# Performance work log

Hardware: AMD Instinct MI355X
Metric: run time of the kernel (lower is better)

The kernel has to match this reference:

```python
import jax, jax.numpy as jnp
import numpy as np

B, S, H = 128, 1000, 256


def setup_inputs() -> dict:
    key = jax.random.key(0)
    ks = jax.random.split(key, 15)
    sc = 1.0 / np.sqrt(H)
    f = lambda k, shape: (jax.random.normal(k, shape, jnp.float32) * sc)
    return dict(
        static_hidden=jax.random.normal(ks[0], (B, S, H), jnp.float32),
        state_embedding=jax.random.normal(ks[1], (B, 1, H), jnp.float32),
        decoder_hidden=jax.random.normal(ks[2], (B, 1, H), jnp.float32),
        target_hidden=jax.random.normal(ks[3], (B, 1, H), jnp.float32),
        last_hh=jax.random.normal(ks[4], (1, B, H), jnp.float32),
        W_ih=f(ks[5], (3 * H, H)),
        W_hh=f(ks[6], (3 * H, H)),
        b_ih=f(ks[7], (3 * H,)),
        b_hh=f(ks[8], (3 * H,)),
        v_attn_enc=f(ks[9], (H,)),
        W_attn_enc=f(ks[10], (H, 2 * H)),
        v_attn_tgt=f(ks[11], (H,)),
        W_attn_tgt=f(ks[12], (H, 2 * H)),
        v_ptr=f(ks[13], (H,)),
        W_ptr=f(ks[14], (H, 3 * H)),
    )


def _attention(static, dec, v, W):
    # static: [B,S,H], dec: [B,1,H] -> softmax attention over S
    hid = jnp.concatenate([static, jnp.broadcast_to(dec, static.shape)], axis=2)  # [B,S,2H]
    t = jnp.tanh(jnp.einsum('hk,bsk->bhs', W, hid))  # [B,H,S]
    return jax.nn.softmax(jnp.einsum('h,bhs->bs', v, t), axis=1)  # [B,S]


def _gru_step(x, h, Wih, Whh, bih, bhh):
    # single-layer single-step torch GRU semantics; x,h: [B,H]
    gi = x @ Wih.T + bih
    gh = h @ Whh.T + bhh
    ir, iz, ig = jnp.split(gi, 3, axis=-1)
    hr, hz, hg = jnp.split(gh, 3, axis=-1)
    r = jax.nn.sigmoid(ir + hr)
    z = jax.nn.sigmoid(iz + hz)
    n = jnp.tanh(ig + r * hg)
    return (1.0 - z) * n + z * h


def _pointer_branch(static, state_emb, attn, v, W):
    context = jnp.einsum('bs,bsh->bh', attn, static)[:, None, :]  # [B,1,H]
    energy = jnp.concatenate(
        [static,
         jnp.broadcast_to(context, static.shape),
         jnp.broadcast_to(state_emb, static.shape)], axis=2)  # [B,S,3H]
    return jnp.einsum('h,bhs->bs', v, jnp.tanh(jnp.einsum('hk,bsk->bhs', W, energy)))


def reference(static_hidden, state_embedding, decoder_hidden, target_hidden, last_hh,
              W_ih, W_hh, b_ih, b_hh,
              v_attn_enc, W_attn_enc, v_attn_tgt, W_attn_tgt, v_ptr, W_ptr):
    # GRU step (dropout is identity in eval / p=0.0)
    h_new = _gru_step(decoder_hidden[:, 0, :], last_hh[0], W_ih, W_hh, b_ih, b_hh)
    rnn_out = h_new[:, None, :]  # [B,1,H]
    last_hh_new = h_new[None]    # [1,B,H]

    enc_attn = _attention(static_hidden, rnn_out, v_attn_enc, W_attn_enc)
    probs = _pointer_branch(static_hidden, state_embedding, enc_attn, v_ptr, W_ptr)

    tgt_attn = _attention(static_hidden, target_hidden, v_attn_tgt, W_attn_tgt)
    # NOTE: original code reuses self.v / self.W (not v_target/W_taret) for the
    # target branch energy -- replicated faithfully.
    probs_target = _pointer_branch(static_hidden, state_embedding, tgt_attn, v_ptr, W_ptr)

    return (5.0 * probs + probs_target, last_hh_new)
```

## Files before the change

kernel.cpp:

```cpp
#include <hip/hip_runtime.h>
#include <hip/hip_bf16.h>
#include <stdint.h>
#include <stddef.h>

#define Bn 128
#define Sn 1000
#define SP 1024
#define Hn 256

typedef __bf16 bf16;
typedef __bf16 bf16x8 __attribute__((ext_vector_type(8)));
typedef __bf16 bf16x4 __attribute__((ext_vector_type(4)));
typedef float  f32x16 __attribute__((ext_vector_type(16)));

typedef __attribute__((address_space(1))) const unsigned int* gas1;
typedef __attribute__((address_space(3))) unsigned int* las3;

__device__ __forceinline__ float fast_tanh(float x){
  return 1.0f - 2.0f / (__expf(2.0f * x) + 1.0f);
}
__device__ __forceinline__ float fast_sigmoid(float x){
  return 1.0f / (1.0f + __expf(-x));
}

__global__ void k0w(const float* __restrict__ We, const float* __restrict__ Wt,
                    const float* __restrict__ Wp, bf16* __restrict__ Wcb,
                    const float* __restrict__ dec, const float* __restrict__ lhh,
                    const float* __restrict__ tgt, const float* __restrict__ se,
                    float* __restrict__ xT, float* __restrict__ hT,
                    float* __restrict__ tT, float* __restrict__ sT){
  int blk = blockIdx.x, t = threadIdx.x;
  if (blk < 768){
    int tt = blk*256 + t;
    int r = tt >> 8, c = tt & 255;
    float val;
    if (r < 256)       val = We[r*512 + c];
    else if (r < 512)  val = Wt[(r-256)*512 + c];
    else               val = Wp[(r-512)*768 + c];
    Wcb[tt] = (bf16)val;
  } else {
    int idx = blk - 768;
    int a = idx >> 7, bb = idx & 127;
    const float* src = (a==0) ? dec : (a==1) ? lhh : (a==2) ? tgt : se;
    float* dst       = (a==0) ? xT  : (a==1) ? hT  : (a==2) ? tT  : sT;
    dst[t*128 + bb] = src[bb*256 + t];
  }
}

__global__ __launch_bounds__(512) void k1a_gru(
    const float* __restrict__ xT, const float* __restrict__ hT,
    const float* __restrict__ Wih, const float* __restrict__ Whh,
    const float* __restrict__ bih, const float* __restrict__ bhh,
    float* __restrict__ out_hh, float* __restrict__ hnT){
  int t = threadIdx.x;
  int g = t >> 7, b = t & 127;
  int h = blockIdx.x*4 + g;
  const float4* wir = (const float4*)(Wih + (size_t)h*256);
  const float4* wiz = (const float4*)(Wih + (size_t)(256+h)*256);
  const float4* wig = (const float4*)(Wih + (size_t)(512+h)*256);
  const float4* whr = (const float4*)(Whh + (size_t)h*256);
  const float4* whz = (const float4*)(Whh + (size_t)(256+h)*256);
  const float4* whg = (const float4*)(Whh + (size_t)(512+h)*256);
  float air=0.f, aiz=0.f, aig=0.f, ahr=0.f, ahz=0.f, ahg=0.f;
  #pragma unroll 2
  for (int kq=0; kq<64; kq++){
    float4 vir = wir[kq], viz = wiz[kq], vig = wig[kq];
    float4 vhr = whr[kq], vhz = whz[kq], vhg = whg[kq];
    #pragma unroll
    for (int e=0;e<4;e++){
      int k = kq*4 + e;
      float xv = xT[k*128 + b];
      float hv = hT[k*128 + b];
      air += (&vir.x)[e]*xv; aiz += (&viz.x)[e]*xv; aig += (&vig.x)[e]*xv;
      ahr += (&vhr.x)[e]*hv; ahz += (&vhz.x)[e]*hv; ahg += (&vhg.x)[e]*hv;
    }
  }
  air += bih[h];      ahr += bhh[h];
  aiz += bih[256+h];  ahz += bhh[256+h];
  aig += bih[512+h];  ahg += bhh[512+h];
  float r = fast_sigmoid(air + ahr);
  float z = fast_sigmoid(aiz + ahz);
  float n = fast_tanh(aig + r*ahg);
  float hprev = hT[h*128 + b];
  float hnew = (1.f - z)*n + z*hprev;
  out_hh[b*256 + h] = hnew;
  hnT[h*128 + b] = hnew;
}

__global__ __launch_bounds__(512) void k1c_dots(
    const float* __restrict__ hnT, const float* __restrict__ tT,
    const float* __restrict__ sT,
    const float* __restrict__ We, const float* __restrict__ Wt,
    const float* __restrict__ Wp,
    float* __restrict__ dEnc, float* __restrict__ dTgt, float* __restrict__ c3){
  int t = threadIdx.x;
  int g = t >> 7, b = t & 127;
  int vr = blockIdx.x*4 + g;
  int var = vr >> 8, h = vr & 255;
  const float* wrow; const float* X; float* dst;
  if (var == 0)      { wrow = We + (size_t)h*512 + 256; X = hnT; dst = dEnc; }
  else if (var == 1) { wrow = Wt + (size_t)h*512 + 256; X = tT;  dst = dTgt; }
  else               { wrow = Wp + (size_t)h*768 + 512; X = sT;  dst = c3; }
  const float4* w4 = (const float4*)wrow;
  float acc = 0.f;
  #pragma unroll 2
  for (int kq=0; kq<64; kq++){
    float4 wv = w4[kq];
    #pragma unroll
    for (int e=0;e<4;e++)
      acc += (&wv.x)[e] * X[(kq*4+e)*128 + b];
  }
  dst[b*256 + h] = acc;
}

__global__ __launch_bounds__(256, 2) void k2_gemm(
    const float* __restrict__ stat, const bf16* __restrict__ Wcb,
    const float* __restrict__ dEnc, const float* __restrict__ dTgt,
    const float* __restrict__ vEnc, const float* __restrict__ vTgt,
    float* __restrict__ scE, float* __restrict__ scT, bf16* __restrict__ Aptr){
  __shared__ __align__(16) bf16 As[64*256];
  __shared__ __align__(16) bf16 Bs[2][256*32];
  __shared__ float scr[2][4][64];
  int tid = threadIdx.x, w = tid>>6, l = tid&63;
  int l31 = l&31, lh = l>>5;
  int st = blockIdx.x, b = blockIdx.y;

  int bnb = w*16 + (l>>2);
  int bg  = l&3;

  {
    int am = tid>>2, agk = tid&3;
    bool aValid = (st*64 + am) < Sn;
    const float4* aSrc4 = (const float4*)(stat + ((size_t)b*Sn + st*64 + am)*Hn);
    #pragma unroll
    for (int i=0;i<8;i++){
      int G = i*4 + agk;
      float4 f0 = make_float4(0.f,0.f,0.f,0.f), f1 = f0;
      if (aValid){ f0 = aSrc4[G*2]; f1 = aSrc4[G*2+1]; }
      bf16x8 v;
      v[0]=(bf16)f0.x; v[1]=(bf16)f0.y; v[2]=(bf16)f0.z; v[3]=(bf16)f0.w;
      v[4]=(bf16)f1.x; v[5]=(bf16)f1.y; v[6]=(bf16)f1.z; v[7]=(bf16)f1.w;
      *(bf16x8*)&As[am*256 + ((G ^ (am&7))<<3)] = v;
    }
  }
  __syncthreads();

#define STAGE(it, buf) { \
  const bf16* wb_ = Wcb + (size_t)((it)>>3)*65536 + ((it)&7)*32; \
  _Pragma("unroll") \
  for (int i_=0;i_<4;i_++){ \
    int n_ = i_*64 + bnb; \
    int g_ = bg ^ ((n_>>1)&3); \
    __builtin_amdgcn_global_load_lds((gas1)(wb_ + (size_t)n_*256 + g_*8), \
        (las3)(&Bs[buf][i_*2048 + w*512]), 16, 0, 0); \
  } }

#define CHUNK(it) { \
  const bf16* bsr_ = &Bs[(it)&1][0]; \
  _Pragma("unroll") \
  for (int ks=0; ks<2; ks++){ \
    int kg_ = ks*2 + lh; \
    int G_ = ((it)&7)*4 + kg_; \
    int sa_ = (G_ ^ (l31&7))<<3; \
    bf16x8 af0 = *(const bf16x8*)&As[l31*256 + sa_]; \
    bf16x8 af1 = *(const bf16x8*)&As[(32+l31)*256 + sa_]; \
    _Pragma("unroll") \
    for (int c_=0;c_<2;c_++){ \
      int n_ = w*64 + c_*32 + l31; \
      bf16x8 wf = *(const bf16x8*)&bsr_[n_*32 + ((kg_ ^ ((n_>>1)&3))<<3)]; \
      acc[0][c_] = __builtin_amdgcn_mfma_f32_32x32x16_bf16(wf, af0, acc[0][c_], 0,0,0); \
      acc[1][c_] = __builtin_amdgcn_mfma_f32_32x32x16_bf16(wf, af1, acc[1][c_], 0,0,0); \
    } \
  } }

  STAGE(0, 0);
  STAGE(1, 1);
  __builtin_amdgcn_sched_barrier(0);
  asm volatile("s_waitcnt vmcnt(4)" ::: "memory");
  __builtin_amdgcn_sched_barrier(0);
  __builtin_amdgcn_s_barrier();
  __builtin_amdgcn_sched_barrier(0);

  float scp0[2] = {0.f,0.f}, scp1[2] = {0.f,0.f};
  f32x16 acc[2][2];

  #pragma unroll
  for (int p=0; p<3; p++){
    #pragma unroll
    for (int a=0;a<2;a++)
      #pragma unroll
      for (int c=0;c<2;c++)
        #pragma unroll
        for (int r=0;r<16;r++) acc[a][c][r] = 0.f;

    #pragma unroll
    for (int kt=0; kt<8; kt++){
      int it = p*8 + kt;
      CHUNK(it);
      if (it < 23){
        __builtin_amdgcn_sched_barrier(0);
        __builtin_amdgcn_s_barrier();
        __builtin_amdgcn_sched_barrier(0);
        if (it < 22){ STAGE(it+2, (it&1)); }
        __builtin_amdgcn_sched_barrier(0);
        if (it < 22){ asm volatile("s_waitcnt vmcnt(4)" ::: "memory"); }
        else        { asm volatile("s_waitcnt vmcnt(0)" ::: "memory"); }
        __builtin_amdgcn_sched_barrier(0);
        __builtin_amdgcn_s_barrier();
        __builtin_amdgcn_sched_barrier(0);
      }
    }

    if (p < 2){
      const float* vv = p ? vTgt : vEnc;
      const float* db = (p ? dTgt : dEnc) + b*256;
      float s0 = 0.f, s1 = 0.f;
      #pragma unroll
      for (int c=0;c<2;c++){
        int nb = w*64 + c*32 + 4*lh;
        #pragma unroll
        for (int r=0;r<16;r++){
          int n = nb + (r&3) + 8*(r>>2);
          float vdv = vv[n], ddv = db[n];
          s0 += vdv * fast_tanh(acc[0][c][r] + ddv);
          s1 += vdv * fast_tanh(acc[1][c][r] + ddv);
        }
      }
      scp0[p] = s0; scp1[p] = s1;
    }
  }

  __syncthreads();
  #pragma unroll
  for (int a=0;a<2;a++){
    int m = a*32 + l31;
    #pragma unroll
    for (int c=0;c<2;c++){
      int g0 = w*8 + c*4 + lh*2;
      bf16x8 lo, hi;
      #pragma unroll
      for (int r=0;r<8;r++){ lo[r] = (bf16)acc[a][c][r]; hi[r] = (bf16)acc[a][c][8+r]; }
      *(bf16x8*)&As[m*256 + (( g0    ^ (m&7))<<3)] = lo;
      *(bf16x8*)&As[m*256 + (((g0+1) ^ (m&7))<<3)] = hi;
    }
  }
  #pragma unroll
  for (int p2=0;p2<2;p2++){
    float v0 = scp0[p2] + __shfl_xor(scp0[p2], 32);
    float v1 = scp1[p2] + __shfl_xor(scp1[p2], 32);
    if (lh == 0){
      scr[p2][w][l31]      = v0;
      scr[p2][w][32 + l31] = v1;
    }
  }
  __syncthreads();
  if (tid < 128){
    int pp = tid>>6, m = tid&63;
    float s = scr[pp][0][m] + scr[pp][1][m] + scr[pp][2][m] + scr[pp][3][m];
    (pp ? scT : scE)[b*SP + st*64 + m] = s;
  }
  {
    int m = tid>>2, part = tid&3;
    bf16* dst = Aptr + ((size_t)(b*1024 + st*64 + m))*256 + part*64;
    #pragma unroll
    for (int i=0;i<8;i++){
      int g = (part*8 + i) ^ (m&7);
      *(bf16x8*)(dst + i*8) = *(const bf16x8*)&As[m*256 + (g<<3)];
    }
  }
#undef STAGE
#undef CHUNK
}

__global__ __launch_bounds__(1024) void k3_ctx(
    const float* __restrict__ scE, const float* __restrict__ scT,
    const float* __restrict__ stat, float* __restrict__ ctxG){
  __shared__ float attE[500], attT[500];
  __shared__ float redE[16], redT[16];
  __shared__ float4 pe4[16][64], pt4[16][64];
  int b = blockIdx.x, sg = blockIdx.y, t = threadIdx.x;
  int wid = t>>6, ln = t&63;

  float vE = (t < Sn) ? scE[b*SP + t] : -1e30f;
  float vT = (t < Sn) ? scT[b*SP + t] : -1e30f;
  float mE = vE, mT = vT;
  #pragma unroll
  for (int o=1;o<64;o<<=1){ mE=fmaxf(mE,__shfl_xor(mE,o)); mT=fmaxf(mT,__shfl_xor(mT,o)); }
  if (ln==0){ redE[wid]=mE; redT[wid]=mT; }
  __syncthreads();
  float ME=-1e30f, MT=-1e30f;
  #pragma unroll
  for (int i=0;i<16;i++){ ME=fmaxf(ME,redE[i]); MT=fmaxf(MT,redT[i]); }
  __syncthreads();
  float eE = (t < Sn) ? __expf(vE-ME) : 0.f;
  float eT = (t < Sn) ? __expf(vT-MT) : 0.f;
  float sE=eE, sT=eT;
  #pragma unroll
  for (int o=1;o<64;o<<=1){ sE+=__shfl_xor(sE,o); sT+=__shfl_xor(sT,o); }
  if (ln==0){ redE[wid]=sE; redT[wid]=sT; }
  __syncthreads();
  float SE=0.f, ST=0.f;
  #pragma unroll
  for (int i=0;i<16;i++){ SE+=redE[i]; ST+=redT[i]; }
  float invE = 1.f/SE, invT = 1.f/ST;
  if (t < 500){
    int s = sg*500 + t;
    attE[t] = __expf(scE[b*SP+s]-ME)*invE;
    attT[t] = __expf(scT[b*SP+s]-MT)*invT;
  }
  __syncthreads();

  int h4 = t & 63, rg = t >> 6;
  float4 aE = make_float4(0.f,0.f,0.f,0.f), aT = aE;
  int nrows = (rg == 15) ? 20 : 32;
  const float4* base = (const float4*)(stat + ((size_t)(b*Sn + sg*500 + rg*32))*Hn) + h4;
  #pragma unroll 4
  for (int i=0;i<nrows;i++){
    float4 f = base[(size_t)i*64];
    float wE = attE[rg*32 + i], wT = attT[rg*32 + i];
    aE.x += wE*f.x; aE.y += wE*f.y; aE.z += wE*f.z; aE.w += wE*f.w;
    aT.x += wT*f.x; aT.y += wT*f.y; aT.z += wT*f.z; aT.w += wT*f.w;
  }
  pe4[rg][h4] = aE; pt4[rg][h4] = aT;
  __syncthreads();
  if (t < 64){
    float4 s = make_float4(0.f,0.f,0.f,0.f);
    #pragma unroll
    for (int i=0;i<16;i++){
      float4 p = pe4[i][t];
      s.x+=p.x; s.y+=p.y; s.z+=p.z; s.w+=p.w;
    }
    atomicAdd(&ctxG[b*256 + t*4 + 0], s.x);
    atomicAdd(&ctxG[b*256 + t*4 + 1], s.y);
    atomicAdd(&ctxG[b*256 + t*4 + 2], s.z);
    atomicAdd(&ctxG[b*256 + t*4 + 3], s.w);
  } else if (t < 128){
    int h = t - 64;
    float4 s = make_float4(0.f,0.f,0.f,0.f);
    #pragma unroll
    for (int i=0;i<16;i++){
      float4 p = pt4[i][h];
      s.x+=p.x; s.y+=p.y; s.z+=p.z; s.w+=p.w;
    }
    atomicAdd(&ctxG[32768 + b*256 + h*4 + 0], s.x);
    atomicAdd(&ctxG[32768 + b*256 + h*4 + 1], s.y);
    atomicAdd(&ctxG[32768 + b*256 + h*4 + 2], s.z);
    atomicAdd(&ctxG[32768 + b*256 + h*4 + 3], s.w);
  }
}

__global__ __launch_bounds__(512) void k3c_c2(
    const float* __restrict__ ctxG, const float* __restrict__ Wp,
    const float* __restrict__ c3,
    float* __restrict__ cE, float* __restrict__ cT){
  __shared__ __align__(16) float ctxL[512];
  int b = blockIdx.x, t = threadIdx.x;
  ctxL[t] = ctxG[(t>>8)*32768 + b*256 + (t&255)];
  __syncthreads();
  int var = t >> 8, h = t & 255;
  const float4* w4 = (const float4*)(Wp + (size_t)h*768 + 256);
  const float4* cv = (const float4*)(&ctxL[var*256]);
  float acc = 0.f;
  #pragma unroll 4
  for (int k=0;k<64;k++){
    float4 wv = w4[k], xv = cv[k];
    acc += wv.x*xv.x + wv.y*xv.y + wv.z*xv.z + wv.w*xv.w;
  }
  (var ? cT : cE)[b*256 + h] = acc + c3[b*256 + h];
}

__global__ __launch_bounds__(256) void k4_final(
    const bf16* __restrict__ Aptr, const float* __restrict__ cE,
    const float* __restrict__ cT, const float* __restrict__ vp,
    float* __restrict__ out){
  int t = threadIdx.x;
  int st = blockIdx.x, b = blockIdx.y;
  int m = t>>2, part = t&3;
  const bf16* src = Aptr + ((size_t)(b*1024 + st*64 + m))*256 + part*64;
  const float* vpb = vp + part*64;
  const float* ceb = cE + b*256 + part*64;
  const float* ctb = cT + b*256 + part*64;
  float pe = 0.f, pt = 0.f;
  #pragma unroll
  for (int i=0;i<8;i++){
    bf16x8 av = *(const bf16x8*)(src + i*8);
    int bi = ((i>>2)<<5) + (((i>>1)&1)<<2) + ((i&1)<<4);
    float4 v0 = *(const float4*)(vpb + bi), v1 = *(const float4*)(vpb + bi + 8);
    float4 e0 = *(const float4*)(ceb + bi), e1 = *(const float4*)(ceb + bi + 8);
    float4 t0 = *(const float4*)(ctb + bi), t1 = *(const float4*)(ctb + bi + 8);
    #pragma unroll
    for (int j=0;j<4;j++){
      float a = (float)av[j];
      pe += (&v0.x)[j] * fast_tanh(a + (&e0.x)[j]);
      pt += (&v0.x)[j] * fast_tanh(a + (&t0.x)[j]);
    }
    #pragma unroll
    for (int j=0;j<4;j++){
      float a = (float)av[4+j];
      pe += (&v1.x)[j] * fast_tanh(a + (&e1.x)[j]);
      pt += (&v1.x)[j] * fast_tanh(a + (&t1.x)[j]);
    }
  }
  pe += __shfl_xor(pe,1); pe += __shfl_xor(pe,2);
  pt += __shfl_xor(pt,1); pt += __shfl_xor(pt,2);
  int s = st*64 + m;
  if (part==0 && s < Sn) out[(size_t)b*Sn + s] = 5.0f*pe + pt;
}

extern "C" void kernel_launch(void* const* d_in, const int* in_sizes, int n_in,
                              void* d_out, int out_size, void* d_ws, size_t ws_size,
                              hipStream_t stream){
  const float* stat = (const float*)d_in[0];
  const float* se   = (const float*)d_in[1];
  const float* dec  = (const float*)d_in[2];
  const float* tgt  = (const float*)d_in[3];
  const float* lhh  = (const float*)d_in[4];
  const float* Wih  = (const float*)d_in[5];
  const float* Whh  = (const float*)d_in[6];
  const float* bih  = (const float*)d_in[7];
  const float* bhh  = (const float*)d_in[8];
  const float* vEnc = (const float*)d_in[9];
  const float* WEnc = (const float*)d_in[10];
  const float* vTgt = (const float*)d_in[11];
  const float* WTgt = (const float*)d_in[12];
  const float* vPtr = (const float*)d_in[13];
  const float* WPtr = (const float*)d_in[14];
  float* out = (float*)d_out;

  char* wsp = (char*)d_ws;
  bf16*  Aptr = (bf16*)(wsp);
  bf16*  Wcb  = (bf16*)(wsp + 67108864);
  float* xT   = (float*)(wsp + 67502080);
  float* hT   = (float*)(wsp + 67633152);
  float* tT   = (float*)(wsp + 67764224);
  float* sT   = (float*)(wsp + 67895296);
  float* hnT  = (float*)(wsp + 68026368);
  float* scE  = (float*)(wsp + 68157440);
  float* scT  = (float*)(wsp + 68681728);
  float* dEnc = (float*)(wsp + 69206016);
  float* dTgt = (float*)(wsp + 69337088);
  float* c3   = (float*)(wsp + 69468160);
  float* cE   = (float*)(wsp + 69599232);
  float* cT   = (float*)(wsp + 69730304);
  float* ctxG = (float*)(wsp + 69861376);

  hipMemsetAsync(ctxG, 0, 262144, stream);
  hipLaunchKernelGGL(k0w, dim3(1280), dim3(256), 0, stream,
                     WEnc, WTgt, WPtr, Wcb, dec, lhh, tgt, se, xT, hT, tT, sT);
  hipLaunchKernelGGL(k1a_gru, dim3(64), dim3(512), 0, stream,
                     xT, hT, Wih, Whh, bih, bhh, out + Bn*Sn, hnT);
  hipLaunchKernelGGL(k1c_dots, dim3(192), dim3(512), 0, stream,
                     hnT, tT, sT, WEnc, WTgt, WPtr, dEnc, dTgt, c3);
  hipLaunchKernelGGL(k2_gemm, dim3(16, 128), dim3(256), 0, stream,
                     stat, Wcb, dEnc, dTgt, vEnc, vTgt, scE, scT, Aptr);
  hipLaunchKernelGGL(k3_ctx, dim3(128, 2), dim3(1024), 0, stream,
                     scE, scT, stat, ctxG);
  hipLaunchKernelGGL(k3c_c2, dim3(128), dim3(512), 0, stream,
                     ctxG, WPtr, c3, cE, cT);
  hipLaunchKernelGGL(k4_final, dim3(16, 128), dim3(256), 0, stream,
                     Aptr, cE, cT, vPtr, out);
}
```

Baseline: 455.2 us.

## Enlarge k2 GEMM tile to 128 rows with 8 waves and 64-wide K chunks

```diff
diff --git a/kernel.cpp b/kernel.cpp
--- a/kernel.cpp
+++ b/kernel.cpp
@@ -113,25 +113,22 @@
   dst[b*256 + h] = acc;
 }
 
-__global__ __launch_bounds__(256, 2) void k2_gemm(
+__global__ __launch_bounds__(512, 2) void k2_gemm(
     const float* __restrict__ stat, const bf16* __restrict__ Wcb,
     const float* __restrict__ dEnc, const float* __restrict__ dTgt,
     const float* __restrict__ vEnc, const float* __restrict__ vTgt,
     float* __restrict__ scE, float* __restrict__ scT, bf16* __restrict__ Aptr){
-  __shared__ __align__(16) bf16 As[64*256];
-  __shared__ __align__(16) bf16 Bs[2][256*32];
-  __shared__ float scr[2][4][64];
+  __shared__ __align__(16) bf16 Bs[2][256*64];
+  __shared__ __align__(16) bf16 As[128*256];
   int tid = threadIdx.x, w = tid>>6, l = tid&63;
   int l31 = l&31, lh = l>>5;
   int st = blockIdx.x, b = blockIdx.y;
-
-  int bnb = w*16 + (l>>2);
-  int bg  = l&3;
+  int wn = (w&3)*64, wm = (w>>2)*64;
 
   {
     int am = tid>>2, agk = tid&3;
-    bool aValid = (st*64 + am) < Sn;
-    const float4* aSrc4 = (const float4*)(stat + ((size_t)b*Sn + st*64 + am)*Hn);
+    bool aValid = (st*128 + am) < Sn;
+    const float4* aSrc4 = (const float4*)(stat + ((size_t)b*Sn + st*128 + am)*Hn);
     #pragma unroll
     for (int i=0;i<8;i++){
       int G = i*4 + agk;
@@ -146,28 +143,28 @@
   __syncthreads();
 
 #define STAGE(it, buf) { \
-  const bf16* wb_ = Wcb + (size_t)((it)>>3)*65536 + ((it)&7)*32; \
+  const bf16* wb_ = Wcb + (size_t)((it)>>2)*65536 + ((it)&3)*64; \
   _Pragma("unroll") \
   for (int i_=0;i_<4;i_++){ \
-    int n_ = i_*64 + bnb; \
-    int g_ = bg ^ ((n_>>1)&3); \
+    int n_ = i_*64 + w*8 + (l>>3); \
+    int g_ = (l&7) ^ (n_&7); \
     __builtin_amdgcn_global_load_lds((gas1)(wb_ + (size_t)n_*256 + g_*8), \
-        (las3)(&Bs[buf][i_*2048 + w*512]), 16, 0, 0); \
+        (las3)(&Bs[buf][(i_*512 + w*64)*8]), 16, 0, 0); \
   } }
 
 #define CHUNK(it) { \
   const bf16* bsr_ = &Bs[(it)&1][0]; \
   _Pragma("unroll") \
-  for (int ks=0; ks<2; ks++){ \
+  for (int ks=0; ks<4; ks++){ \
     int kg_ = ks*2 + lh; \
-    int G_ = ((it)&7)*4 + kg_; \
+    int G_  = ((it)&3)*8 + kg_; \
     int sa_ = (G_ ^ (l31&7))<<3; \
-    bf16x8 af0 = *(const bf16x8*)&As[l31*256 + sa_]; \
-    bf16x8 af1 = *(const bf16x8*)&As[(32+l31)*256 + sa_]; \
+    bf16x8 af0 = *(const bf16x8*)&As[(wm + l31)*256 + sa_]; \
+    bf16x8 af1 = *(const bf16x8*)&As[(wm + 32 + l31)*256 + sa_]; \
     _Pragma("unroll") \
     for (int c_=0;c_<2;c_++){ \
-      int n_ = w*64 + c_*32 + l31; \
-      bf16x8 wf = *(const bf16x8*)&bsr_[n_*32 + ((kg_ ^ ((n_>>1)&3))<<3)]; \
+      int n_ = wn + c_*32 + l31; \
+      bf16x8 wf = *(const bf16x8*)&bsr_[n_*64 + ((kg_ ^ (n_&7))<<3)]; \
       acc[0][c_] = __builtin_amdgcn_mfma_f32_32x32x16_bf16(wf, af0, acc[0][c_], 0,0,0); \
       acc[1][c_] = __builtin_amdgcn_mfma_f32_32x32x16_bf16(wf, af1, acc[1][c_], 0,0,0); \
     } \
@@ -194,16 +191,16 @@
         for (int r=0;r<16;r++) acc[a][c][r] = 0.f;
 
     #pragma unroll
-    for (int kt=0; kt<8; kt++){
-      int it = p*8 + kt;
+    for (int kt=0; kt<4; kt++){
+      int it = p*4 + kt;
       CHUNK(it);
-      if (it < 23){
+      if (it < 11){
         __builtin_amdgcn_sched_barrier(0);
         __builtin_amdgcn_s_barrier();
         __builtin_amdgcn_sched_barrier(0);
-        if (it < 22){ STAGE(it+2, (it&1)); }
+        if (it < 10){ STAGE(it+2, (it&1)); }
         __builtin_amdgcn_sched_barrier(0);
-        if (it < 22){ asm volatile("s_waitcnt vmcnt(4)" ::: "memory"); }
+        if (it < 10){ asm volatile("s_waitcnt vmcnt(4)" ::: "memory"); }
         else        { asm volatile("s_waitcnt vmcnt(0)" ::: "memory"); }
         __builtin_amdgcn_sched_barrier(0);
         __builtin_amdgcn_s_barrier();
@@ -217,7 +214,7 @@
       float s0 = 0.f, s1 = 0.f;
       #pragma unroll
       for (int c=0;c<2;c++){
-        int nb = w*64 + c*32 + 4*lh;
+        int nb = wn + c*32 + 4*lh;
         #pragma unroll
         for (int r=0;r<16;r++){
           int n = nb + (r&3) + 8*(r>>2);
@@ -230,13 +227,14 @@
     }
   }
 
+  float (*scr)[8][64] = (float (*)[8][64])&Bs[0][0];
   __syncthreads();
   #pragma unroll
   for (int a=0;a<2;a++){
-    int m = a*32 + l31;
+    int m = wm + a*32 + l31;
     #pragma unroll
     for (int c=0;c<2;c++){
-      int g0 = w*8 + c*4 + lh*2;
+      int g0 = (w&3)*8 + c*4 + lh*2;
       bf16x8 lo, hi;
       #pragma unroll
       for (int r=0;r<8;r++){ lo[r] = (bf16)acc[a][c][r]; hi[r] = (bf16)acc[a][c][8+r]; }
@@ -254,14 +252,16 @@
     }
   }
   __syncthreads();
-  if (tid < 128){
-    int pp = tid>>6, m = tid&63;
-    float s = scr[pp][0][m] + scr[pp][1][m] + scr[pp][2][m] + scr[pp][3][m];
-    (pp ? scT : scE)[b*SP + st*64 + m] = s;
+  if (tid < 256){
+    int pp = tid>>7, m = tid&127;
+    int grp = (m>>6)*4, mi = m&63;
+    float s = scr[pp][grp][mi] + scr[pp][grp+1][mi]
+            + scr[pp][grp+2][mi] + scr[pp][grp+3][mi];
+    (pp ? scT : scE)[b*SP + st*128 + m] = s;
   }
   {
     int m = tid>>2, part = tid&3;
-    bf16* dst = Aptr + ((size_t)(b*1024 + st*64 + m))*256 + part*64;
+    bf16* dst = Aptr + (((size_t)(b*8 + st)*128 + m))*256 + part*64;
     #pragma unroll
     for (int i=0;i<8;i++){
       int g = (part*8 + i) ^ (m&7);
@@ -369,14 +369,14 @@
   (var ? cT : cE)[b*256 + h] = acc + c3[b*256 + h];
 }
 
-__global__ __launch_bounds__(256) void k4_final(
+__global__ __launch_bounds__(512) void k4_final(
     const bf16* __restrict__ Aptr, const float* __restrict__ cE,
     const float* __restrict__ cT, const float* __restrict__ vp,
     float* __restrict__ out){
   int t = threadIdx.x;
   int st = blockIdx.x, b = blockIdx.y;
   int m = t>>2, part = t&3;
-  const bf16* src = Aptr + ((size_t)(b*1024 + st*64 + m))*256 + part*64;
+  const bf16* src = Aptr + (((size_t)(b*8 + st)*128 + m))*256 + part*64;
   const float* vpb = vp + part*64;
   const float* ceb = cE + b*256 + part*64;
   const float* ctb = cT + b*256 + part*64;
@@ -403,7 +403,7 @@
   }
   pe += __shfl_xor(pe,1); pe += __shfl_xor(pe,2);
   pt += __shfl_xor(pt,1); pt += __shfl_xor(pt,2);
-  int s = st*64 + m;
+  int s = st*128 + m;
   if (part==0 && s < Sn) out[(size_t)b*Sn + s] = 5.0f*pe + pt;
 }
 
@@ -451,12 +451,12 @@
                      xT, hT, Wih, Whh, bih, bhh, out + Bn*Sn, hnT);
   hipLaunchKernelGGL(k1c_dots, dim3(192), dim3(512), 0, stream,
                      hnT, tT, sT, WEnc, WTgt, WPtr, dEnc, dTgt, c3);
-  hipLaunchKernelGGL(k2_gemm, dim3(16, 128), dim3(256), 0, stream,
+  hipLaunchKernelGGL(k2_gemm, dim3(8, 128), dim3(512), 0, stream,
                      stat, Wcb, dEnc, dTgt, vEnc, vTgt, scE, scT, Aptr);
   hipLaunchKernelGGL(k3_ctx, dim3(128, 2), dim3(1024), 0, stream,
                      scE, scT, stat, ctxG);
   hipLaunchKernelGGL(k3c_c2, dim3(128), dim3(512), 0, stream,
                      ctxG, WPtr, c3, cE, cT);
-  hipLaunchKernelGGL(k4_final, dim3(16, 128), dim3(256), 0, stream,
+  hipLaunchKernelGGL(k4_final, dim3(8, 128), dim3(512), 0, stream,
                      Aptr, cE, cT, vPtr, out);
 }
```

After: 475.2 us. 4.4% more time.

## Triple-buffer weight tiles with interleaved loads and MFMA priority; split context kernel finer

Applied to the files above, without the earlier changes.

```diff
diff --git a/kernel.cpp b/kernel.cpp
--- a/kernel.cpp
+++ b/kernel.cpp
@@ -118,12 +118,12 @@
     const float* __restrict__ dEnc, const float* __restrict__ dTgt,
     const float* __restrict__ vEnc, const float* __restrict__ vTgt,
     float* __restrict__ scE, float* __restrict__ scT, bf16* __restrict__ Aptr){
+  __shared__ __align__(16) bf16 Bs[3][256*32];
   __shared__ __align__(16) bf16 As[64*256];
-  __shared__ __align__(16) bf16 Bs[2][256*32];
-  __shared__ float scr[2][4][64];
   int tid = threadIdx.x, w = tid>>6, l = tid&63;
   int l31 = l&31, lh = l>>5;
   int st = blockIdx.x, b = blockIdx.y;
+  int wn = w*64;
 
   int bnb = w*16 + (l>>2);
   int bg  = l&3;
@@ -145,41 +145,17 @@
   }
   __syncthreads();
 
-#define STAGE(it, buf) { \
+#define BISSUE(it, i_) { \
   const bf16* wb_ = Wcb + (size_t)((it)>>3)*65536 + ((it)&7)*32; \
-  _Pragma("unroll") \
-  for (int i_=0;i_<4;i_++){ \
-    int n_ = i_*64 + bnb; \
-    int g_ = bg ^ ((n_>>1)&3); \
-    __builtin_amdgcn_global_load_lds((gas1)(wb_ + (size_t)n_*256 + g_*8), \
-        (las3)(&Bs[buf][i_*2048 + w*512]), 16, 0, 0); \
-  } }
-
-#define CHUNK(it) { \
-  const bf16* bsr_ = &Bs[(it)&1][0]; \
-  _Pragma("unroll") \
-  for (int ks=0; ks<2; ks++){ \
-    int kg_ = ks*2 + lh; \
-    int G_ = ((it)&7)*4 + kg_; \
-    int sa_ = (G_ ^ (l31&7))<<3; \
-    bf16x8 af0 = *(const bf16x8*)&As[l31*256 + sa_]; \
-    bf16x8 af1 = *(const bf16x8*)&As[(32+l31)*256 + sa_]; \
-    _Pragma("unroll") \
-    for (int c_=0;c_<2;c_++){ \
-      int n_ = w*64 + c_*32 + l31; \
-      bf16x8 wf = *(const bf16x8*)&bsr_[n_*32 + ((kg_ ^ ((n_>>1)&3))<<3)]; \
-      acc[0][c_] = __builtin_amdgcn_mfma_f32_32x32x16_bf16(wf, af0, acc[0][c_], 0,0,0); \
-      acc[1][c_] = __builtin_amdgcn_mfma_f32_32x32x16_bf16(wf, af1, acc[1][c_], 0,0,0); \
-    } \
-  } }
-
-  STAGE(0, 0);
-  STAGE(1, 1);
-  __builtin_amdgcn_sched_barrier(0);
+  int n_ = (i_)*64 + bnb; \
+  int g_ = bg ^ ((n_>>1)&3); \
+  __builtin_amdgcn_global_load_lds((gas1)(wb_ + (size_t)n_*256 + g_*8), \
+      (las3)(&Bs[(it)%3][(i_)*2048 + w*512]), 16, 0, 0); }
+
+  BISSUE(0,0); BISSUE(0,1); BISSUE(0,2); BISSUE(0,3);
+  BISSUE(1,0); BISSUE(1,1); BISSUE(1,2); BISSUE(1,3);
   asm volatile("s_waitcnt vmcnt(4)" ::: "memory");
-  __builtin_amdgcn_sched_barrier(0);
   __builtin_amdgcn_s_barrier();
-  __builtin_amdgcn_sched_barrier(0);
 
   float scp0[2] = {0.f,0.f}, scp1[2] = {0.f,0.f};
   f32x16 acc[2][2];
@@ -196,18 +172,32 @@
     #pragma unroll
     for (int kt=0; kt<8; kt++){
       int it = p*8 + kt;
-      CHUNK(it);
-      if (it < 23){
+      const bf16* bsr = &Bs[it%3][0];
+      #pragma unroll
+      for (int sp=0; sp<2; sp++){
+        int kg = sp*2 + lh;
+        int G  = kt*4 + kg;
+        int sa = (G ^ (l31&7))<<3;
+        bf16x8 af0 = *(const bf16x8*)&As[l31*256 + sa];
+        bf16x8 af1 = *(const bf16x8*)&As[(32+l31)*256 + sa];
+        int n0 = wn + l31, n1 = wn + 32 + l31;
+        bf16x8 wf0 = *(const bf16x8*)&bsr[n0*32 + ((kg ^ ((n0>>1)&3))<<3)];
+        bf16x8 wf1 = *(const bf16x8*)&bsr[n1*32 + ((kg ^ ((n1>>1)&3))<<3)];
+        if (it < 22){ BISSUE(it+2, sp*2); BISSUE(it+2, sp*2+1); }
+        if (sp == 1){
+          if (it < 22){ asm volatile("s_waitcnt vmcnt(4)" ::: "memory"); }
+          else        { asm volatile("s_waitcnt vmcnt(0)" ::: "memory"); }
+        }
+        __builtin_amdgcn_s_barrier();
+        asm volatile("s_waitcnt lgkmcnt(0)" ::: "memory");
         __builtin_amdgcn_sched_barrier(0);
+        __builtin_amdgcn_s_setprio(1);
+        acc[0][0] = __builtin_amdgcn_mfma_f32_32x32x16_bf16(wf0, af0, acc[0][0], 0,0,0);
+        acc[1][0] = __builtin_amdgcn_mfma_f32_32x32x16_bf16(wf0, af1, acc[1][0], 0,0,0);
+        acc[0][1] = __builtin_amdgcn_mfma_f32_32x32x16_bf16(wf1, af0, acc[0][1], 0,0,0);
+        acc[1][1] = __builtin_amdgcn_mfma_f32_32x32x16_bf16(wf1, af1, acc[1][1], 0,0,0);
+        __builtin_amdgcn_s_setprio(0);
         __builtin_amdgcn_s_barrier();
-        __builtin_amdgcn_sched_barrier(0);
-        if (it < 22){ STAGE(it+2, (it&1)); }
-        __builtin_amdgcn_sched_barrier(0);
-        if (it < 22){ asm volatile("s_waitcnt vmcnt(4)" ::: "memory"); }
-        else        { asm volatile("s_waitcnt vmcnt(0)" ::: "memory"); }
-        __builtin_amdgcn_sched_barrier(0);
-        __builtin_amdgcn_s_barrier();
-        __builtin_amdgcn_sched_barrier(0);
       }
     }
 
@@ -217,7 +207,7 @@
       float s0 = 0.f, s1 = 0.f;
       #pragma unroll
       for (int c=0;c<2;c++){
-        int nb = w*64 + c*32 + 4*lh;
+        int nb = wn + c*32 + 4*lh;
         #pragma unroll
         for (int r=0;r<16;r++){
           int n = nb + (r&3) + 8*(r>>2);
@@ -230,6 +220,7 @@
     }
   }
 
+  float (*scr)[4][64] = (float (*)[4][64])&Bs[0][0];
   __syncthreads();
   #pragma unroll
   for (int a=0;a<2;a++){
@@ -268,14 +259,13 @@
       *(bf16x8*)(dst + i*8) = *(const bf16x8*)&As[m*256 + (g<<3)];
     }
   }
-#undef STAGE
-#undef CHUNK
+#undef BISSUE
 }
 
 __global__ __launch_bounds__(1024) void k3_ctx(
     const float* __restrict__ scE, const float* __restrict__ scT,
     const float* __restrict__ stat, float* __restrict__ ctxG){
-  __shared__ float attE[500], attT[500];
+  __shared__ float attE[250], attT[250];
   __shared__ float redE[16], redT[16];
   __shared__ float4 pe4[16][64], pt4[16][64];
   int b = blockIdx.x, sg = blockIdx.y, t = threadIdx.x;
@@ -303,8 +293,8 @@
   #pragma unroll
   for (int i=0;i<16;i++){ SE+=redE[i]; ST+=redT[i]; }
   float invE = 1.f/SE, invT = 1.f/ST;
-  if (t < 500){
-    int s = sg*500 + t;
+  if (t < 250){
+    int s = sg*250 + t;
     attE[t] = __expf(scE[b*SP+s]-ME)*invE;
     attT[t] = __expf(scT[b*SP+s]-MT)*invT;
   }
@@ -312,12 +302,12 @@
 
   int h4 = t & 63, rg = t >> 6;
   float4 aE = make_float4(0.f,0.f,0.f,0.f), aT = aE;
-  int nrows = (rg == 15) ? 20 : 32;
-  const float4* base = (const float4*)(stat + ((size_t)(b*Sn + sg*500 + rg*32))*Hn) + h4;
+  int nrows = (rg == 15) ? 10 : 16;
+  const float4* base = (const float4*)(stat + ((size_t)(b*Sn + sg*250 + rg*16))*Hn) + h4;
   #pragma unroll 4
   for (int i=0;i<nrows;i++){
     float4 f = base[(size_t)i*64];
-    float wE = attE[rg*32 + i], wT = attT[rg*32 + i];
+    float wE = attE[rg*16 + i], wT = attT[rg*16 + i];
     aE.x += wE*f.x; aE.y += wE*f.y; aE.z += wE*f.z; aE.w += wE*f.w;
     aT.x += wT*f.x; aT.y += wT*f.y; aT.z += wT*f.z; aT.w += wT*f.w;
   }
@@ -453,7 +443,7 @@
                      hnT, tT, sT, WEnc, WTgt, WPtr, dEnc, dTgt, c3);
   hipLaunchKernelGGL(k2_gemm, dim3(16, 128), dim3(256), 0, stream,
                      stat, Wcb, dEnc, dTgt, vEnc, vTgt, scE, scT, Aptr);
-  hipLaunchKernelGGL(k3_ctx, dim3(128, 2), dim3(1024), 0, stream,
+  hipLaunchKernelGGL(k3_ctx, dim3(128, 4), dim3(1024), 0, stream,
                      scE, scT, stat, ctxG);
   hipLaunchKernelGGL(k3c_c2, dim3(128), dim3(512), 0, stream,
                      ctxG, WPtr, c3, cE, cT);
```

Result: no change. 462.6 us (+1.6%).
